# Kernel tuning notes

Measured on AMD Instinct MI355X. Metric: run time of the kernel, lower is better.

Reference implementation:

```python
import jax, jax.numpy as jnp
import numpy as np

EPS = 1e-5

def setup_inputs() -> dict:
    key = jax.random.key(0)
    ks = jax.random.split(key, 16)
    n_users, n_items, d = 100000, 50000, 128
    n_nodes = n_users + n_items
    E = 4800000
    B = 16384
    h1, h2 = 256, 128
    xavier = lambda k, shp: jax.random.uniform(k, shp, jnp.float32, -1.0, 1.0) * np.sqrt(6.0 / (shp[0] + shp[1]))
    inp = {
        'user_indices': jax.random.randint(ks[0], (B,), 0, n_users),
        'item_indices': jax.random.randint(ks[1], (B,), 0, n_items),
        'edge_rows': jax.random.randint(ks[2], (E,), 0, n_nodes, dtype=jnp.int32),
        'edge_cols': jax.random.randint(ks[3], (E,), 0, n_nodes, dtype=jnp.int32),
        'edge_vals': jax.random.uniform(ks[4], (E,), jnp.float32),
        'user_emb': xavier(ks[5], (n_users, d)),
        'item_emb': xavier(ks[6], (n_items, d)),
        'W1': xavier(ks[7], (d, h1)), 'b1': jnp.zeros((h1,), jnp.float32),
        'g1': jnp.ones((h1,), jnp.float32), 'beta1': jnp.zeros((h1,), jnp.float32),
        'W2': xavier(ks[8], (h1, h2)), 'b2': jnp.zeros((h2,), jnp.float32),
        'g2': jnp.ones((h2,), jnp.float32), 'beta2': jnp.zeros((h2,), jnp.float32),
        'P1': xavier(ks[9], (2 * h2, h2)), 'pb1': jnp.zeros((h2,), jnp.float32),
        'P2': xavier(ks[10], (h2, 1)), 'pb2': jnp.zeros((1,), jnp.float32),
    }
    return inp

def _gcn_layer(x, rows, cols, vals, n_nodes, W, b, g, beta):
    # linear transform then sparse adjacency aggregation (COO):
    # out[r] = sum_{e: rows[e]==r} vals[e] * t[cols[e]]
    t = x @ W + b                                   # [N, out]
    agg = jax.ops.segment_sum(vals[:, None] * t[cols], rows, num_segments=n_nodes)
    # BatchNorm1d (training-mode batch statistics over nodes)
    mu = jnp.mean(agg, axis=0)
    var = jnp.var(agg, axis=0)
    out = (agg - mu) * jax.lax.rsqrt(var + EPS) * g + beta
    return jax.nn.relu(out)                         # dropout = identity (eval)

def reference(user_indices, item_indices, edge_rows, edge_cols, edge_vals,
              user_emb, item_emb, W1, b1, g1, beta1, W2, b2, g2, beta2,
              P1, pb1, P2, pb2):
    n_users = user_emb.shape[0]
    x = jnp.concatenate([user_emb, item_emb], axis=0)  # [N, d]
    n_nodes = x.shape[0]
    x = _gcn_layer(x, edge_rows, edge_cols, edge_vals, n_nodes, W1, b1, g1, beta1)
    x = _gcn_layer(x, edge_rows, edge_cols, edge_vals, n_nodes, W2, b2, g2, beta2)
    u = x[:n_users][user_indices]                      # [B, h2]
    v = x[n_users:][item_indices]                      # [B, h2]
    combined = jnp.concatenate([u, v], axis=-1)        # [B, 2*h2]
    h = jax.nn.relu(combined @ P1 + pb1)
    pred = (h @ P2 + pb2).squeeze(-1)                  # [B]
    return pred
```

## Files before the change

### kernel.cpp

```cpp
#include <hip/hip_runtime.h>
#include <stdint.h>

#define N_USERS 100000
#define N_NODES 150000
#define D0      128
#define H1      256
#define H2      128
#define NEDGE   4800000
#define BATCH   16384
#define EPSV    1e-5f
#define NBUCK   147
#define BCHUNK  4096
#define CCHUNK  16384

typedef short short8  __attribute__((ext_vector_type(8)));
typedef float floatx4 __attribute__((ext_vector_type(4)));
typedef unsigned short u16;

__device__ inline float bf2f(u16 u) {
    union { float f; uint32_t i; } x; x.i = ((uint32_t)u) << 16; return x.f;
}
__device__ inline u16 f2bf(float f) {
    union { float f; uint32_t i; } x; x.f = f;
    return (u16)((x.i + 0x7FFFu + ((x.i >> 16) & 1u)) >> 16);
}
__device__ inline float itof(uint32_t u) {
    union { float f; uint32_t i; } x; x.i = u; return x.f;
}
__device__ inline uint32_t ftoi(float f) {
    union { float f; uint32_t i; } x; x.f = f; return x.i;
}
__device__ inline uint32_t pack2(float a, float b) {
    return (uint32_t)f2bf(a) | ((uint32_t)f2bf(b) << 16);
}

__global__ __launch_bounds__(256) void k_init(float* __restrict__ out, int out_n,
                                              int* __restrict__ bcount,
                                              float* __restrict__ stats1,
                                              float* __restrict__ stats2) {
    int i = blockIdx.x * 256 + threadIdx.x;
    if (i < out_n) out[i] = 2.0f;
    if (i < NBUCK + 1) bcount[i] = 0;
    if (i < 2 * H1) stats1[i] = 0.f;
    if (i < 2 * H2) stats2[i] = 0.f;
}

__global__ __launch_bounds__(256) void k_cvt(const float* __restrict__ ue,
                                             const float* __restrict__ ie,
                                             u16* __restrict__ xb) {
    int i = (blockIdx.x * 256 + threadIdx.x) * 4;
    const int NU = N_USERS * D0;
    const int NT = N_NODES * D0;
    if (i >= NT) return;
    const float* src = (i < NU) ? (ue + i) : (ie + (i - NU));
    float4 f = *(const float4*)(const void*)src;
    uint2 w;
    w.x = pack2(f.x, f.y);
    w.y = pack2(f.z, f.w);
    *(uint2*)(void*)(xb + i) = w;
}

__global__ __launch_bounds__(256) void k_bcount(const int* __restrict__ rows,
                                                int* __restrict__ bcount) {
    __shared__ int h[NBUCK];
    int tid = threadIdx.x;
    for (int i = tid; i < NBUCK; i += 256) h[i] = 0;
    __syncthreads();
    int e0 = blockIdx.x * CCHUNK;
    int nE = NEDGE - e0; if (nE > CCHUNK) nE = CCHUNK;
    for (int i = tid; i < nE; i += 256) atomicAdd(&h[rows[e0 + i] >> 10], 1);
    __syncthreads();
    for (int i = tid; i < NBUCK; i += 256)
        if (h[i] > 0) atomicAdd(&bcount[i], h[i]);
}

__global__ __launch_bounds__(256) void k_bscan(const int* __restrict__ bcount,
                                               int* __restrict__ bucket_base,
                                               int* __restrict__ bucket_cursor,
                                               int* __restrict__ row_ptr) {
    int tid = threadIdx.x;
    int c = (tid < NBUCK) ? bcount[tid] : 0;
    int lane = tid & 63, wid = tid >> 6;
    int v = c;
    for (int off = 1; off < 64; off <<= 1) {
        int u = __shfl_up(v, off, 64);
        if (lane >= off) v += u;
    }
    __shared__ int wsum[4];
    if (lane == 63) wsum[wid] = v;
    __syncthreads();
    if (tid == 0) {
        int acc = 0;
        for (int w = 0; w < 4; ++w) { int t = wsum[w]; wsum[w] = acc; acc += t; }
    }
    __syncthreads();
    int ex = wsum[wid] + (v - c);
    if (tid < NBUCK) { bucket_base[tid] = ex; bucket_cursor[tid] = ex; }
    if (tid == 0) { bucket_base[NBUCK] = NEDGE; row_ptr[N_NODES] = NEDGE; }
}

__global__ __launch_bounds__(256) void k_bucket(const int* __restrict__ rows,
                                                const int* __restrict__ cols,
                                                const float* __restrict__ vals,
                                                int* __restrict__ bucket_cursor,
                                                uint2* __restrict__ etmp) {
    __shared__ uint2 stage[BCHUNK];
    __shared__ u16   slotb[BCHUNK];
    __shared__ int   lcnt[NBUCK + 1];
    __shared__ int   lscan[NBUCK + 1];
    __shared__ int   gstart[NBUCK];
    __shared__ int   wsum[4];
    int tid = threadIdx.x;
    int e0 = blockIdx.x * BCHUNK;
    int nE = NEDGE - e0; if (nE > BCHUNK) nE = BCHUNK;

    for (int i = tid; i <= NBUCK; i += 256) lcnt[i] = 0;
    __syncthreads();
    for (int i = tid; i < nE; i += 256) atomicAdd(&lcnt[rows[e0 + i] >> 10], 1);
    __syncthreads();
    int c = (tid < NBUCK) ? lcnt[tid] : 0;
    if (tid < NBUCK) gstart[tid] = atomicAdd(&bucket_cursor[tid], c);
    {
        int lane = tid & 63, wid = tid >> 6;
        int v = c;
        for (int off = 1; off < 64; off <<= 1) {
            int u = __shfl_up(v, off, 64);
            if (lane >= off) v += u;
        }
        if (lane == 63) wsum[wid] = v;
        __syncthreads();
        if (tid == 0) {
            int acc = 0;
            for (int w = 0; w < 4; ++w) { int t = wsum[w]; wsum[w] = acc; acc += t; }
        }
        __syncthreads();
        if (tid < NBUCK) lscan[tid] = wsum[wid] + (v - c);
        for (int i = tid; i < NBUCK; i += 256) lcnt[i] = 0;
    }
    __syncthreads();
    for (int i = tid; i < nE; i += 256) {
        int r = rows[e0 + i];
        int b = r >> 10;
        int lidx = atomicAdd(&lcnt[b], 1);
        int slot = lscan[b] + lidx;
        uint2 p;
        p.x = ((uint32_t)(r & 1023) << 18) | (uint32_t)cols[e0 + i];
        p.y = ftoi(vals[e0 + i]);
        stage[slot] = p;
        slotb[slot] = (u16)b;
    }
    __syncthreads();
    for (int s = tid; s < nE; s += 256) {
        int b = slotb[s];
        etmp[gstart[b] + (s - lscan[b])] = stage[s];
    }
}

__global__ __launch_bounds__(1024) void k_place2(const int* __restrict__ bucket_base,
                                                 const uint2* __restrict__ etmp,
                                                 int* __restrict__ row_ptr,
                                                 uint2* __restrict__ efin) {
    __shared__ int lcnt[1024];
    __shared__ int lcur[1024];
    __shared__ int wsum[16];
    int b = blockIdx.x;
    int tid = threadIdx.x;
    int base = b << 10;
    int bstart = bucket_base[b];
    int bend   = bucket_base[b + 1];
    lcnt[tid] = 0;
    __syncthreads();
    for (int i = bstart + tid; i < bend; i += 1024)
        atomicAdd(&lcnt[etmp[i].x >> 18], 1);
    __syncthreads();
    int c = lcnt[tid];
    int lane = tid & 63, wid = tid >> 6;
    int v = c;
    for (int off = 1; off < 64; off <<= 1) {
        int u = __shfl_up(v, off, 64);
        if (lane >= off) v += u;
    }
    if (lane == 63) wsum[wid] = v;
    __syncthreads();
    if (tid == 0) {
        int acc = 0;
        for (int w = 0; w < 16; ++w) { int t = wsum[w]; wsum[w] = acc; acc += t; }
    }
    __syncthreads();
    int ex = wsum[wid] + (v - c);
    int gpos = bstart + ex;
    if (base + tid < N_NODES) row_ptr[base + tid] = gpos;
    lcur[tid] = gpos;
    __syncthreads();
    for (int i = bstart + tid; i < bend; i += 1024) {
        uint2 p = etmp[i];
        int rl = (int)(p.x >> 18);
        int pos = atomicAdd(&lcur[rl], 1);
        uint2 o; o.x = p.x & 0x3FFFFu; o.y = p.y;
        efin[pos] = o;
    }
}

__global__ __launch_bounds__(256) void k_transpose3(const float* __restrict__ W1,
                                                    const float* __restrict__ W2,
                                                    const float* __restrict__ P1,
                                                    u16* __restrict__ WT1,
                                                    u16* __restrict__ WT2,
                                                    u16* __restrict__ PT1) {
    int gi = blockIdx.x * 256 + threadIdx.x;
    int seg = gi >> 15;
    int i = gi & 32767;
    const float* W; u16* WT; int K, N;
    if (seg == 0)      { W = W1; WT = WT1; K = D0;     N = H1; }
    else if (seg == 1) { W = W2; WT = WT2; K = H1;     N = H2; }
    else               { W = P1; WT = PT1; K = 2 * H2; N = H2; }
    int k = i / N, n = i - k * N;
    WT[n * K + k] = f2bf(W[i]);
}

__global__ __launch_bounds__(256) void k_gemm(const u16* __restrict__ A, int M, int K,
                                              const u16* __restrict__ BT,
                                              const float* __restrict__ bias,
                                              const float* __restrict__ rowscale,
                                              u16* __restrict__ C, int N, int relu) {
    __shared__ u16 lbt[64 * 264];
    int tid = threadIdx.x;
    int lane = tid & 63, wid = tid >> 6;
    int m0 = blockIdx.x * 64;
    int n0 = blockIdx.y * 64;
    const int KP = K + 8;
    int cpr = K / 8;
    for (int idx = tid; idx < 64 * cpr; idx += 256) {
        int r = idx / cpr, c = idx - r * cpr;
        *(uint4*)(void*)(lbt + r * KP + c * 8) =
            *(const uint4*)(const void*)(BT + (size_t)(n0 + r) * K + c * 8);
    }
    __syncthreads();
    int rn = lane & 15;
    int kq = (lane >> 4) * 8;
    int mrow = m0 + wid * 16 + rn;
    int mclamp = mrow < M ? mrow : M - 1;
    const u16* aptr = A + (size_t)mclamp * K + kq;
    floatx4 acc0 = {0.f,0.f,0.f,0.f}, acc1 = acc0, acc2 = acc0, acc3 = acc0;
    for (int kt = 0; kt < K; kt += 32) {
        short8 a  = *(const short8*)(const void*)(aptr + kt);
        short8 b0 = *(const short8*)(const void*)(lbt + ( 0 + rn) * KP + kq + kt);
        short8 b1 = *(const short8*)(const void*)(lbt + (16 + rn) * KP + kq + kt);
        short8 b2 = *(const short8*)(const void*)(lbt + (32 + rn) * KP + kq + kt);
        short8 b3 = *(const short8*)(const void*)(lbt + (48 + rn) * KP + kq + kt);
        acc0 = __builtin_amdgcn_mfma_f32_16x16x32_bf16(a, b0, acc0, 0, 0, 0);
        acc1 = __builtin_amdgcn_mfma_f32_16x16x32_bf16(a, b1, acc1, 0, 0, 0);
        acc2 = __builtin_amdgcn_mfma_f32_16x16x32_bf16(a, b2, acc2, 0, 0, 0);
        acc3 = __builtin_amdgcn_mfma_f32_16x16x32_bf16(a, b3, acc3, 0, 0, 0);
    }
    int rbase = m0 + wid * 16 + (lane >> 4) * 4;
    floatx4 accs[4] = {acc0, acc1, acc2, acc3};
    for (int j = 0; j < 4; ++j) {
        int col = n0 + j * 16 + rn;
        float bs = bias[col];
        for (int i = 0; i < 4; ++i) {
            int row = rbase + i;
            if (row < M) {
                float rs = rowscale ? rowscale[row] : 1.0f;
                float v = accs[j][i] + rs * bs;
                if (relu) v = v < 0.f ? 0.f : v;
                C[(size_t)row * N + col] = f2bf(v);
            }
        }
    }
}

__device__ inline void accum8(float* acc, uint4 r, float v) {
    acc[0] += v * bf2f((u16)(r.x & 0xffffu)); acc[1] += v * bf2f((u16)(r.x >> 16));
    acc[2] += v * bf2f((u16)(r.y & 0xffffu)); acc[3] += v * bf2f((u16)(r.y >> 16));
    acc[4] += v * bf2f((u16)(r.z & 0xffffu)); acc[5] += v * bf2f((u16)(r.z >> 16));
    acc[6] += v * bf2f((u16)(r.w & 0xffffu)); acc[7] += v * bf2f((u16)(r.w >> 16));
}

__global__ __launch_bounds__(256) void k_agg(const u16* __restrict__ t,
                                             const int* __restrict__ row_ptr,
                                             const uint2* __restrict__ edges,
                                             u16* __restrict__ agg,
                                             float* __restrict__ rowsum) {
    int tid = threadIdx.x;
    int lane = tid & 63;
    int sub = lane >> 4;
    int l16 = lane & 15;
    int row = blockIdx.x * 16 + (tid >> 6) * 4 + sub;
    float acc[8] = {0.f,0.f,0.f,0.f,0.f,0.f,0.f,0.f};
    float sv = 0.f;
    int s = row_ptr[row], e = row_ptr[row + 1];
    const u16* tf = t + l16 * 8;
    int i = s;
    for (; i + 4 <= e; i += 4) {
        uint2 e0 = edges[i], e1 = edges[i+1], e2 = edges[i+2], e3 = edges[i+3];
        uint4 r0 = *(const uint4*)(const void*)(tf + (size_t)e0.x * 128);
        uint4 r1 = *(const uint4*)(const void*)(tf + (size_t)e1.x * 128);
        uint4 r2 = *(const uint4*)(const void*)(tf + (size_t)e2.x * 128);
        uint4 r3 = *(const uint4*)(const void*)(tf + (size_t)e3.x * 128);
        float v0 = itof(e0.y), v1 = itof(e1.y), v2 = itof(e2.y), v3 = itof(e3.y);
        accum8(acc, r0, v0); accum8(acc, r1, v1);
        accum8(acc, r2, v2); accum8(acc, r3, v3);
        sv += v0 + v1 + v2 + v3;
    }
    for (; i < e; ++i) {
        uint2 e0 = edges[i];
        uint4 r0 = *(const uint4*)(const void*)(tf + (size_t)e0.x * 128);
        float v0 = itof(e0.y);
        accum8(acc, r0, v0);
        sv += v0;
    }
    uint4 w;
    w.x = pack2(acc[0], acc[1]); w.y = pack2(acc[2], acc[3]);
    w.z = pack2(acc[4], acc[5]); w.w = pack2(acc[6], acc[7]);
    *(uint4*)(void*)(agg + (size_t)row * 128 + l16 * 8) = w;
    if (rowsum != nullptr && l16 == 0) rowsum[row] = sv;
}

__global__ __launch_bounds__(256) void k_bnstats(const u16* __restrict__ agg,
                                                 float* __restrict__ stats, int NF) {
    int tid = threadIdx.x;
    int rpb = 256 / NF;
    int f = tid & (NF - 1);
    int r0 = blockIdx.x * rpb + tid / NF;
    int rs = gridDim.x * rpb;
    float s = 0.f, s2 = 0.f;
    for (int row = r0; row < N_NODES; row += rs) {
        float v = bf2f(agg[(size_t)row * NF + f]);
        s += v; s2 += v * v;
    }
    atomicAdd(&stats[f], s);
    atomicAdd(&stats[NF + f], s2);
}

__global__ __launch_bounds__(256) void k_bnapply(const u16* __restrict__ agg,
                                                 const float* __restrict__ stats,
                                                 const float* __restrict__ g,
                                                 const float* __restrict__ beta,
                                                 u16* __restrict__ x, int NF) {
    size_t idx = (size_t)blockIdx.x * 256 + threadIdx.x;
    if (idx >= (size_t)N_NODES * NF) return;
    int f = (int)(idx & (size_t)(NF - 1));
    float mu = stats[f] * (1.0f / N_NODES);
    float var = stats[NF + f] * (1.0f / N_NODES) - mu * mu;
    float sc = rsqrtf(var + EPSV) * g[f];
    float v = (bf2f(agg[idx]) - mu) * sc + beta[f];
    x[idx] = f2bf(v < 0.f ? 0.f : v);
}

__global__ __launch_bounds__(256) void k_gatherBN(const int* __restrict__ ui,
                                                  const int* __restrict__ ii,
                                                  const u16* __restrict__ agg2,
                                                  const float* __restrict__ stats,
                                                  const float* __restrict__ g,
                                                  const float* __restrict__ beta,
                                                  u16* __restrict__ comb) {
    int item = blockIdx.x * 4 + (threadIdx.x >> 6);
    int lane = threadIdx.x & 63;
    if (item >= BATCH) return;
    int node = (lane < 32) ? ui[item] : (N_USERS + ii[item]);
    int fb = (lane & 31) * 4;
    uint2 r = *(const uint2*)(const void*)(agg2 + (size_t)node * H2 + fb);
    float vv[4] = { bf2f((u16)(r.x & 0xffffu)), bf2f((u16)(r.x >> 16)),
                    bf2f((u16)(r.y & 0xffffu)), bf2f((u16)(r.y >> 16)) };
    u16 o[4];
    for (int j = 0; j < 4; ++j) {
        int f = fb + j;
        float mu = stats[f] * (1.0f / N_NODES);
        float var = stats[H2 + f] * (1.0f / N_NODES) - mu * mu;
        float sc = rsqrtf(var + EPSV) * g[f];
        float v = (vv[j] - mu) * sc + beta[f];
        o[j] = f2bf(v < 0.f ? 0.f : v);
    }
    uint2 w;
    w.x = (uint32_t)o[0] | ((uint32_t)o[1] << 16);
    w.y = (uint32_t)o[2] | ((uint32_t)o[3] << 16);
    *(uint2*)(void*)(comb + (size_t)item * (2 * H2) + lane * 4) = w;
}

__global__ __launch_bounds__(256) void k_final(const u16* __restrict__ h,
                                               const float* __restrict__ P2,
                                               const float* __restrict__ pb2,
                                               float* __restrict__ out) {
    int item = blockIdx.x * 4 + (threadIdx.x >> 6);
    int lane = threadIdx.x & 63;
    if (item >= BATCH) return;
    float a = bf2f(h[(size_t)item * H2 + lane])      * P2[lane]
            + bf2f(h[(size_t)item * H2 + 64 + lane]) * P2[64 + lane];
    for (int off = 32; off > 0; off >>= 1) a += __shfl_down(a, off, 64);
    if (lane == 0) out[item] = a + pb2[0];
}

extern "C" void kernel_launch(void* const* d_in, const int* in_sizes, int n_in,
                              void* d_out, int out_size, void* d_ws, size_t ws_size,
                              hipStream_t stream) {
    (void)in_sizes; (void)n_in; (void)ws_size;
    const int* user_indices = (const int*)d_in[0];
    const int* item_indices = (const int*)d_in[1];
    const int* edge_rows    = (const int*)d_in[2];
    const int* edge_cols    = (const int*)d_in[3];
    const float* edge_vals = (const float*)d_in[4];
    const float* user_emb  = (const float*)d_in[5];
    const float* item_emb  = (const float*)d_in[6];
    const float* W1    = (const float*)d_in[7];
    const float* b1    = (const float*)d_in[8];
    const float* g1    = (const float*)d_in[9];
    const float* beta1 = (const float*)d_in[10];
    const float* W2    = (const float*)d_in[11];
    const float* b2    = (const float*)d_in[12];
    const float* g2    = (const float*)d_in[13];
    const float* beta2 = (const float*)d_in[14];
    const float* P1    = (const float*)d_in[15];
    const float* pb1   = (const float*)d_in[16];
    const float* P2    = (const float*)d_in[17];
    const float* pb2   = (const float*)d_in[18];
    float* out = (float*)d_out;

    char* ws = (char*)d_ws;
    size_t off = 0;
    auto alloc = [&](size_t bytes) -> char* {
        char* p = ws + off;
        off = (off + bytes + 255) & ~(size_t)255;
        return p;
    };
    int*   row_ptr  = (int*)alloc(sizeof(int) * (N_NODES + 1));
    int*   bcount   = (int*)alloc(sizeof(int) * (NBUCK + 1));
    int*   bbase    = (int*)alloc(sizeof(int) * (NBUCK + 1));
    int*   bcursor  = (int*)alloc(sizeof(int) * (NBUCK + 1));
    float* rowsum   = (float*)alloc(sizeof(float) * N_NODES);
    float* stats1   = (float*)alloc(sizeof(float) * 2 * H1);
    float* stats2   = (float*)alloc(sizeof(float) * 2 * H2);
    u16* WT1 = (u16*)alloc(2 * D0 * H1);
    u16* WT2 = (u16*)alloc(2 * H1 * H2);
    u16* PT1 = (u16*)alloc(2 * 2 * H2 * H2);
    uint2* efin = (uint2*)alloc(8 * (size_t)NEDGE);
    u16* R1   = (u16*)alloc(2 * (size_t)N_NODES * H1);
    u16* xb   = R1;
    u16* aggx = R1 + (size_t)N_NODES * D0;
    u16* x1   = R1;
    u16* R2   = (u16*)alloc(2 * (size_t)N_NODES * H1);
    uint2* etmp = (uint2*)R2;
    u16* agg1 = R2;
    u16* t2   = R2;
    u16* agg2 = R2 + (size_t)N_NODES * H2;
    u16* comb = R2;
    u16* hbuf = R2 + (size_t)BATCH * 2 * H2;

    k_init<<<(out_size + 255) / 256, 256, 0, stream>>>(out, out_size, bcount, stats1, stats2);

    k_cvt<<<(N_NODES * D0 / 4 + 255) / 256, 256, 0, stream>>>(user_emb, item_emb, xb);

    k_bcount<<<(NEDGE + CCHUNK - 1) / CCHUNK, 256, 0, stream>>>(edge_rows, bcount);
    k_bscan<<<1, 256, 0, stream>>>(bcount, bbase, bcursor, row_ptr);
    k_bucket<<<(NEDGE + BCHUNK - 1) / BCHUNK, 256, 0, stream>>>(
        edge_rows, edge_cols, edge_vals, bcursor, etmp);
    k_place2<<<NBUCK, 1024, 0, stream>>>(bbase, etmp, row_ptr, efin);

    k_transpose3<<<(3 * 32768) / 256, 256, 0, stream>>>(W1, W2, P1, WT1, WT2, PT1);

    k_agg<<<N_NODES / 16, 256, 0, stream>>>(xb, row_ptr, efin, aggx, rowsum);
    k_gemm<<<dim3((N_NODES + 63) / 64, H1 / 64), 256, 0, stream>>>(
        aggx, N_NODES, D0, WT1, b1, rowsum, agg1, H1, 0);
    k_bnstats<<<512, 256, 0, stream>>>(agg1, stats1, H1);
    k_bnapply<<<(N_NODES * H1) / 256, 256, 0, stream>>>(agg1, stats1, g1, beta1, x1, H1);

    k_gemm<<<dim3((N_NODES + 63) / 64, H2 / 64), 256, 0, stream>>>(
        x1, N_NODES, H1, WT2, b2, nullptr, t2, H2, 0);
    k_agg<<<N_NODES / 16, 256, 0, stream>>>(t2, row_ptr, efin, agg2, nullptr);
    k_bnstats<<<512, 256, 0, stream>>>(agg2, stats2, H2);

    k_gatherBN<<<BATCH / 4, 256, 0, stream>>>(user_indices, item_indices, agg2,
                                              stats2, g2, beta2, comb);
    k_gemm<<<dim3(BATCH / 64, H2 / 64), 256, 0, stream>>>(
        comb, BATCH, 2 * H2, PT1, pb1, nullptr, hbuf, H2, 1);
    k_final<<<BATCH / 4, 256, 0, stream>>>(hbuf, P2, pb2, out);
}
```

Measured before the change: 1.018 ms.

## Fuse layer-1 BatchNorm stats into GEMM epilogue and apply into next GEMM

Layer-1 BatchNorm statistics are now gathered as per-block partial column sums in the first GEMM's epilogue, then reduced by a small finalize kernel into per-feature scale and shift. The second GEMM applies that scale/shift plus ReLU to its A operand as it loads it. This removes the separate stats pass and the normalize pass over the 150000x256 activation. Nontemporal loads and stores are also added in the edge bucketing, placement and aggregation kernels. The trade-off is extra per-element ALU in the GEMM inner loop, and statistics computed from fp32 values before bf16 rounding.

```diff
diff --git a/kernel.cpp b/kernel.cpp
--- a/kernel.cpp
+++ b/kernel.cpp
@@ -15,6 +15,8 @@
 
 typedef short short8  __attribute__((ext_vector_type(8)));
 typedef float floatx4 __attribute__((ext_vector_type(4)));
+typedef unsigned int uint2e __attribute__((ext_vector_type(2)));
+typedef unsigned int uint4e __attribute__((ext_vector_type(4)));
 typedef unsigned short u16;
 
 __device__ inline float bf2f(u16 u) {
@@ -36,12 +38,10 @@
 
 __global__ __launch_bounds__(256) void k_init(float* __restrict__ out, int out_n,
                                               int* __restrict__ bcount,
-                                              float* __restrict__ stats1,
                                               float* __restrict__ stats2) {
     int i = blockIdx.x * 256 + threadIdx.x;
     if (i < out_n) out[i] = 2.0f;
     if (i < NBUCK + 1) bcount[i] = 0;
-    if (i < 2 * H1) stats1[i] = 0.f;
     if (i < 2 * H2) stats2[i] = 0.f;
 }
 
@@ -54,10 +54,10 @@
     if (i >= NT) return;
     const float* src = (i < NU) ? (ue + i) : (ie + (i - NU));
     float4 f = *(const float4*)(const void*)src;
-    uint2 w;
+    uint2e w;
     w.x = pack2(f.x, f.y);
     w.y = pack2(f.z, f.w);
-    *(uint2*)(void*)(xb + i) = w;
+    *(uint2e*)(void*)(xb + i) = w;
 }
 
 __global__ __launch_bounds__(256) void k_bcount(const int* __restrict__ rows,
@@ -103,8 +103,9 @@
                                                 const int* __restrict__ cols,
                                                 const float* __restrict__ vals,
                                                 int* __restrict__ bucket_cursor,
-                                                uint2* __restrict__ etmp) {
-    __shared__ uint2 stage[BCHUNK];
+                                                uint2e* __restrict__ etmp) {
+    __shared__ uint32_t stx[BCHUNK];
+    __shared__ uint32_t sty[BCHUNK];
     __shared__ u16   slotb[BCHUNK];
     __shared__ int   lcnt[NBUCK + 1];
     __shared__ int   lscan[NBUCK + 1];
@@ -143,23 +144,23 @@
         int b = r >> 10;
         int lidx = atomicAdd(&lcnt[b], 1);
         int slot = lscan[b] + lidx;
-        uint2 p;
-        p.x = ((uint32_t)(r & 1023) << 18) | (uint32_t)cols[e0 + i];
-        p.y = ftoi(vals[e0 + i]);
-        stage[slot] = p;
+        stx[slot] = ((uint32_t)(r & 1023) << 18) |
+                    (uint32_t)__builtin_nontemporal_load(&cols[e0 + i]);
+        sty[slot] = ftoi(__builtin_nontemporal_load(&vals[e0 + i]));
         slotb[slot] = (u16)b;
     }
     __syncthreads();
     for (int s = tid; s < nE; s += 256) {
         int b = slotb[s];
-        etmp[gstart[b] + (s - lscan[b])] = stage[s];
+        uint2e p; p.x = stx[s]; p.y = sty[s];
+        __builtin_nontemporal_store(p, &etmp[gstart[b] + (s - lscan[b])]);
     }
 }
 
 __global__ __launch_bounds__(1024) void k_place2(const int* __restrict__ bucket_base,
-                                                 const uint2* __restrict__ etmp,
+                                                 const uint2e* __restrict__ etmp,
                                                  int* __restrict__ row_ptr,
-                                                 uint2* __restrict__ efin) {
+                                                 uint2e* __restrict__ efin) {
     __shared__ int lcnt[1024];
     __shared__ int lcur[1024];
     __shared__ int wsum[16];
@@ -193,11 +194,11 @@
     lcur[tid] = gpos;
     __syncthreads();
     for (int i = bstart + tid; i < bend; i += 1024) {
-        uint2 p = etmp[i];
+        uint2e p = __builtin_nontemporal_load(&etmp[i]);
         int rl = (int)(p.x >> 18);
         int pos = atomicAdd(&lcur[rl], 1);
-        uint2 o; o.x = p.x & 0x3FFFFu; o.y = p.y;
-        efin[pos] = o;
+        uint2e o; o.x = p.x & 0x3FFFFu; o.y = p.y;
+        __builtin_nontemporal_store(o, &efin[pos]);
     }
 }
 
@@ -222,8 +223,13 @@
                                               const u16* __restrict__ BT,
                                               const float* __restrict__ bias,
                                               const float* __restrict__ rowscale,
+                                              const float* __restrict__ bnm,
+                                              const float* __restrict__ bna,
+                                              float2* __restrict__ pstat,
                                               u16* __restrict__ C, int N, int relu) {
     __shared__ u16 lbt[64 * 264];
+    __shared__ float lbnm[256], lbna[256];
+    __shared__ float colstat[64][2];
     int tid = threadIdx.x;
     int lane = tid & 63, wid = tid >> 6;
     int m0 = blockIdx.x * 64;
@@ -232,9 +238,13 @@
     int cpr = K / 8;
     for (int idx = tid; idx < 64 * cpr; idx += 256) {
         int r = idx / cpr, c = idx - r * cpr;
-        *(uint4*)(void*)(lbt + r * KP + c * 8) =
-            *(const uint4*)(const void*)(BT + (size_t)(n0 + r) * K + c * 8);
-    }
+        *(uint4e*)(void*)(lbt + r * KP + c * 8) =
+            *(const uint4e*)(const void*)(BT + (size_t)(n0 + r) * K + c * 8);
+    }
+    if (bnm) {
+        for (int i = tid; i < K; i += 256) { lbnm[i] = bnm[i]; lbna[i] = bna[i]; }
+    }
+    if (pstat && tid < 128) ((float*)colstat)[tid] = 0.f;
     __syncthreads();
     int rn = lane & 15;
     int kq = (lane >> 4) * 8;
@@ -244,6 +254,14 @@
     floatx4 acc0 = {0.f,0.f,0.f,0.f}, acc1 = acc0, acc2 = acc0, acc3 = acc0;
     for (int kt = 0; kt < K; kt += 32) {
         short8 a  = *(const short8*)(const void*)(aptr + kt);
+        if (bnm) {
+            int kb = kq + kt;
+            #pragma unroll
+            for (int e = 0; e < 8; ++e) {
+                float v = bf2f((u16)a[e]) * lbnm[kb + e] + lbna[kb + e];
+                a[e] = (short)f2bf(v < 0.f ? 0.f : v);
+            }
+        }
         short8 b0 = *(const short8*)(const void*)(lbt + ( 0 + rn) * KP + kq + kt);
         short8 b1 = *(const short8*)(const void*)(lbt + (16 + rn) * KP + kq + kt);
         short8 b2 = *(const short8*)(const void*)(lbt + (32 + rn) * KP + kq + kt);
@@ -258,6 +276,7 @@
     for (int j = 0; j < 4; ++j) {
         int col = n0 + j * 16 + rn;
         float bs = bias[col];
+        float s1 = 0.f, s2 = 0.f;
         for (int i = 0; i < 4; ++i) {
             int row = rbase + i;
             if (row < M) {
@@ -265,12 +284,60 @@
                 float v = accs[j][i] + rs * bs;
                 if (relu) v = v < 0.f ? 0.f : v;
                 C[(size_t)row * N + col] = f2bf(v);
+                s1 += v; s2 += v * v;
             }
         }
-    }
-}
-
-__device__ inline void accum8(float* acc, uint4 r, float v) {
+        if (pstat) {
+            s1 += __shfl_down(s1, 32, 64); s1 += __shfl_down(s1, 16, 64);
+            s2 += __shfl_down(s2, 32, 64); s2 += __shfl_down(s2, 16, 64);
+            if (lane < 16) {
+                atomicAdd(&colstat[j * 16 + lane][0], s1);
+                atomicAdd(&colstat[j * 16 + lane][1], s2);
+            }
+        }
+    }
+    if (pstat) {
+        __syncthreads();
+        if (tid < 64) {
+            float2 o; o.x = colstat[tid][0]; o.y = colstat[tid][1];
+            pstat[((size_t)blockIdx.y * gridDim.x + blockIdx.x) * 64 + tid] = o;
+        }
+    }
+}
+
+__global__ __launch_bounds__(256) void k_bnfin(const float2* __restrict__ pstat, int GX,
+                                               const float* __restrict__ g,
+                                               const float* __restrict__ beta,
+                                               float* __restrict__ bnmul,
+                                               float* __restrict__ bnadd) {
+    int f = blockIdx.x;
+    int by = f >> 6, cl = f & 63;
+    int tid = threadIdx.x;
+    float s = 0.f, s2 = 0.f;
+    for (int bx = tid; bx < GX; bx += 256) {
+        float2 p = pstat[((size_t)by * GX + bx) * 64 + cl];
+        s += p.x; s2 += p.y;
+    }
+    for (int off = 32; off > 0; off >>= 1) {
+        s += __shfl_down(s, off, 64);
+        s2 += __shfl_down(s2, off, 64);
+    }
+    __shared__ float ws[4][2];
+    int lane = tid & 63, wid = tid >> 6;
+    if (lane == 0) { ws[wid][0] = s; ws[wid][1] = s2; }
+    __syncthreads();
+    if (tid == 0) {
+        float ts  = ws[0][0] + ws[1][0] + ws[2][0] + ws[3][0];
+        float ts2 = ws[0][1] + ws[1][1] + ws[2][1] + ws[3][1];
+        float mu = ts * (1.0f / N_NODES);
+        float var = ts2 * (1.0f / N_NODES) - mu * mu;
+        float sc = rsqrtf(var + EPSV) * g[f];
+        bnmul[f] = sc;
+        bnadd[f] = beta[f] - mu * sc;
+    }
+}
+
+__device__ inline void accum8(float* acc, uint4e r, float v) {
     acc[0] += v * bf2f((u16)(r.x & 0xffffu)); acc[1] += v * bf2f((u16)(r.x >> 16));
     acc[2] += v * bf2f((u16)(r.y & 0xffffu)); acc[3] += v * bf2f((u16)(r.y >> 16));
     acc[4] += v * bf2f((u16)(r.z & 0xffffu)); acc[5] += v * bf2f((u16)(r.z >> 16));
@@ -279,7 +346,7 @@
 
 __global__ __launch_bounds__(256) void k_agg(const u16* __restrict__ t,
                                              const int* __restrict__ row_ptr,
-                                             const uint2* __restrict__ edges,
+                                             const uint2e* __restrict__ edges,
                                              u16* __restrict__ agg,
                                              float* __restrict__ rowsum) {
     int tid = threadIdx.x;
@@ -293,27 +360,30 @@
     const u16* tf = t + l16 * 8;
     int i = s;
     for (; i + 4 <= e; i += 4) {
-        uint2 e0 = edges[i], e1 = edges[i+1], e2 = edges[i+2], e3 = edges[i+3];
-        uint4 r0 = *(const uint4*)(const void*)(tf + (size_t)e0.x * 128);
-        uint4 r1 = *(const uint4*)(const void*)(tf + (size_t)e1.x * 128);
-        uint4 r2 = *(const uint4*)(const void*)(tf + (size_t)e2.x * 128);
-        uint4 r3 = *(const uint4*)(const void*)(tf + (size_t)e3.x * 128);
+        uint2e e0 = __builtin_nontemporal_load(&edges[i]);
+        uint2e e1 = __builtin_nontemporal_load(&edges[i + 1]);
+        uint2e e2 = __builtin_nontemporal_load(&edges[i + 2]);
+        uint2e e3 = __builtin_nontemporal_load(&edges[i + 3]);
+        uint4e r0 = *(const uint4e*)(const void*)(tf + (size_t)e0.x * 128);
+        uint4e r1 = *(const uint4e*)(const void*)(tf + (size_t)e1.x * 128);
+        uint4e r2 = *(const uint4e*)(const void*)(tf + (size_t)e2.x * 128);
+        uint4e r3 = *(const uint4e*)(const void*)(tf + (size_t)e3.x * 128);
         float v0 = itof(e0.y), v1 = itof(e1.y), v2 = itof(e2.y), v3 = itof(e3.y);
         accum8(acc, r0, v0); accum8(acc, r1, v1);
         accum8(acc, r2, v2); accum8(acc, r3, v3);
         sv += v0 + v1 + v2 + v3;
     }
     for (; i < e; ++i) {
-        uint2 e0 = edges[i];
-        uint4 r0 = *(const uint4*)(const void*)(tf + (size_t)e0.x * 128);
+        uint2e e0 = __builtin_nontemporal_load(&edges[i]);
+        uint4e r0 = *(const uint4e*)(const void*)(tf + (size_t)e0.x * 128);
         float v0 = itof(e0.y);
         accum8(acc, r0, v0);
         sv += v0;
     }
-    uint4 w;
+    uint4e w;
     w.x = pack2(acc[0], acc[1]); w.y = pack2(acc[2], acc[3]);
     w.z = pack2(acc[4], acc[5]); w.w = pack2(acc[6], acc[7]);
-    *(uint4*)(void*)(agg + (size_t)row * 128 + l16 * 8) = w;
+    __builtin_nontemporal_store(w, (uint4e*)(void*)(agg + (size_t)row * 128 + l16 * 8));
     if (rowsum != nullptr && l16 == 0) rowsum[row] = sv;
 }
 
@@ -331,21 +401,6 @@
     }
     atomicAdd(&stats[f], s);
     atomicAdd(&stats[NF + f], s2);
-}
-
-__global__ __launch_bounds__(256) void k_bnapply(const u16* __restrict__ agg,
-                                                 const float* __restrict__ stats,
-                                                 const float* __restrict__ g,
-                                                 const float* __restrict__ beta,
-                                                 u16* __restrict__ x, int NF) {
-    size_t idx = (size_t)blockIdx.x * 256 + threadIdx.x;
-    if (idx >= (size_t)N_NODES * NF) return;
-    int f = (int)(idx & (size_t)(NF - 1));
-    float mu = stats[f] * (1.0f / N_NODES);
-    float var = stats[NF + f] * (1.0f / N_NODES) - mu * mu;
-    float sc = rsqrtf(var + EPSV) * g[f];
-    float v = (bf2f(agg[idx]) - mu) * sc + beta[f];
-    x[idx] = f2bf(v < 0.f ? 0.f : v);
 }
 
 __global__ __launch_bounds__(256) void k_gatherBN(const int* __restrict__ ui,
@@ -360,7 +415,7 @@
     if (item >= BATCH) return;
     int node = (lane < 32) ? ui[item] : (N_USERS + ii[item]);
     int fb = (lane & 31) * 4;
-    uint2 r = *(const uint2*)(const void*)(agg2 + (size_t)node * H2 + fb);
+    uint2e r = *(const uint2e*)(const void*)(agg2 + (size_t)node * H2 + fb);
     float vv[4] = { bf2f((u16)(r.x & 0xffffu)), bf2f((u16)(r.x >> 16)),
                     bf2f((u16)(r.y & 0xffffu)), bf2f((u16)(r.y >> 16)) };
     u16 o[4];
@@ -372,10 +427,10 @@
         float v = (vv[j] - mu) * sc + beta[f];
         o[j] = f2bf(v < 0.f ? 0.f : v);
     }
-    uint2 w;
+    uint2e w;
     w.x = (uint32_t)o[0] | ((uint32_t)o[1] << 16);
     w.y = (uint32_t)o[2] | ((uint32_t)o[3] << 16);
-    *(uint2*)(void*)(comb + (size_t)item * (2 * H2) + lane * 4) = w;
+    *(uint2e*)(void*)(comb + (size_t)item * (2 * H2) + lane * 4) = w;
 }
 
 __global__ __launch_bounds__(256) void k_final(const u16* __restrict__ h,
@@ -416,6 +471,8 @@
     const float* pb2   = (const float*)d_in[18];
     float* out = (float*)d_out;
 
+    const int GX1 = (N_NODES + 63) / 64;
+
     char* ws = (char*)d_ws;
     size_t off = 0;
     auto alloc = [&](size_t bytes) -> char* {
@@ -428,25 +485,26 @@
     int*   bbase    = (int*)alloc(sizeof(int) * (NBUCK + 1));
     int*   bcursor  = (int*)alloc(sizeof(int) * (NBUCK + 1));
     float* rowsum   = (float*)alloc(sizeof(float) * N_NODES);
-    float* stats1   = (float*)alloc(sizeof(float) * 2 * H1);
     float* stats2   = (float*)alloc(sizeof(float) * 2 * H2);
+    float* bnm1     = (float*)alloc(sizeof(float) * H1);
+    float* bna1     = (float*)alloc(sizeof(float) * H1);
+    float2* pstat   = (float2*)alloc(sizeof(float2) * 4 * (size_t)GX1 * 64);
     u16* WT1 = (u16*)alloc(2 * D0 * H1);
     u16* WT2 = (u16*)alloc(2 * H1 * H2);
     u16* PT1 = (u16*)alloc(2 * 2 * H2 * H2);
-    uint2* efin = (uint2*)alloc(8 * (size_t)NEDGE);
+    uint2e* efin = (uint2e*)alloc(8 * (size_t)NEDGE);
     u16* R1   = (u16*)alloc(2 * (size_t)N_NODES * H1);
     u16* xb   = R1;
     u16* aggx = R1 + (size_t)N_NODES * D0;
-    u16* x1   = R1;
+    u16* t2   = R1;
+    u16* agg2 = R1 + (size_t)N_NODES * D0;
     u16* R2   = (u16*)alloc(2 * (size_t)N_NODES * H1);
-    uint2* etmp = (uint2*)R2;
+    uint2e* etmp = (uint2e*)R2;
     u16* agg1 = R2;
-    u16* t2   = R2;
-    u16* agg2 = R2 + (size_t)N_NODES * H2;
     u16* comb = R2;
     u16* hbuf = R2 + (size_t)BATCH * 2 * H2;
 
-    k_init<<<(out_size + 255) / 256, 256, 0, stream>>>(out, out_size, bcount, stats1, stats2);
+    k_init<<<(out_size + 255) / 256, 256, 0, stream>>>(out, out_size, bcount, stats2);
 
     k_cvt<<<(N_NODES * D0 / 4 + 255) / 256, 256, 0, stream>>>(user_emb, item_emb, xb);
 
@@ -459,19 +517,18 @@
     k_transpose3<<<(3 * 32768) / 256, 256, 0, stream>>>(W1, W2, P1, WT1, WT2, PT1);
 
     k_agg<<<N_NODES / 16, 256, 0, stream>>>(xb, row_ptr, efin, aggx, rowsum);
-    k_gemm<<<dim3((N_NODES + 63) / 64, H1 / 64), 256, 0, stream>>>(
-        aggx, N_NODES, D0, WT1, b1, rowsum, agg1, H1, 0);
-    k_bnstats<<<512, 256, 0, stream>>>(agg1, stats1, H1);
-    k_bnapply<<<(N_NODES * H1) / 256, 256, 0, stream>>>(agg1, stats1, g1, beta1, x1, H1);
-
-    k_gemm<<<dim3((N_NODES + 63) / 64, H2 / 64), 256, 0, stream>>>(
-        x1, N_NODES, H1, WT2, b2, nullptr, t2, H2, 0);
+    k_gemm<<<dim3(GX1, H1 / 64), 256, 0, stream>>>(
+        aggx, N_NODES, D0, WT1, b1, rowsum, nullptr, nullptr, pstat, agg1, H1, 0);
+    k_bnfin<<<H1, 256, 0, stream>>>(pstat, GX1, g1, beta1, bnm1, bna1);
+
+    k_gemm<<<dim3(GX1, H2 / 64), 256, 0, stream>>>(
+        agg1, N_NODES, H1, WT2, b2, nullptr, bnm1, bna1, nullptr, t2, H2, 0);
     k_agg<<<N_NODES / 16, 256, 0, stream>>>(t2, row_ptr, efin, agg2, nullptr);
     k_bnstats<<<512, 256, 0, stream>>>(agg2, stats2, H2);
 
     k_gatherBN<<<BATCH / 4, 256, 0, stream>>>(user_indices, item_indices, agg2,
                                               stats2, g2, beta2, comb);
     k_gemm<<<dim3(BATCH / 64, H2 / 64), 256, 0, stream>>>(
-        comb, BATCH, 2 * H2, PT1, pb1, nullptr, hbuf, H2, 1);
+        comb, BATCH, 2 * H2, PT1, pb1, nullptr, nullptr, nullptr, nullptr, hbuf, H2, 1);
     k_final<<<BATCH / 4, 256, 0, stream>>>(hbuf, P2, pb2, out);
 }
```

Result: slower. 1.091 ms (+7.2%).
